# Performance work log

Measured on AMD Instinct MI355X. Metric: run time of the kernel, lower is better.

Reference implementation:

```python
import jax, jax.numpy as jnp
import numpy as np

HID = 1024
VOCAB = 50257
MAXLEN = 2048


def setup_inputs() -> dict:
    key = jax.random.key(0)
    ks = jax.random.split(key, 12)
    s = 0.02
    return {
        "input_tok": jax.random.randint(ks[0], (1,), 0, VOCAB),
        "hidden": jax.random.normal(ks[1], (1, 1, HID), jnp.float32),
        "encoder_outputs": jax.random.normal(ks[2], (MAXLEN, HID), jnp.float32),
        "emb": jax.random.normal(ks[3], (VOCAB, HID), jnp.float32) * s,
        "attn_W": jax.random.normal(ks[4], (MAXLEN, 2 * HID), jnp.float32) * s,
        "attn_b": jnp.zeros((MAXLEN,), jnp.float32),
        "comb_W": jax.random.normal(ks[5], (HID, 2 * HID), jnp.float32) * s,
        "comb_b": jnp.zeros((HID,), jnp.float32),
        "W_ih": jax.random.normal(ks[6], (3 * HID, HID), jnp.float32) * s,
        "W_hh": jax.random.normal(ks[7], (3 * HID, HID), jnp.float32) * s,
        "b_ih": jnp.zeros((3 * HID,), jnp.float32),
        "b_hh": jnp.zeros((3 * HID,), jnp.float32),
        "out_W": jax.random.normal(ks[8], (VOCAB, HID), jnp.float32) * s,
        "out_b": jnp.zeros((VOCAB,), jnp.float32),
    }


def reference(input_tok, hidden, encoder_outputs, emb, attn_W, attn_b,
              comb_W, comb_b, W_ih, W_hh, b_ih, b_hh, out_W, out_b):
    H = hidden.shape[-1]
    # embedding lookup -> [1, H]; dropout is identity in eval mode
    embedded = emb[input_tok].reshape(1, H)
    h = hidden[0]  # [1, H]
    # Bahdanau-style attention over fixed max_length
    attn_weights = jax.nn.softmax(
        jnp.concatenate([embedded, h], axis=1) @ attn_W.T + attn_b, axis=1)  # [1, L]
    attn_applied = attn_weights @ encoder_outputs  # [1, H]
    x = jnp.concatenate([embedded, attn_applied], axis=1) @ comb_W.T + comb_b
    x = jax.nn.relu(x)  # [1, H]
    # single GRU step (PyTorch gate layout: r, z, n)
    gi = x @ W_ih.T + b_ih
    gh = h @ W_hh.T + b_hh
    gi_r, gi_z, gi_n = jnp.split(gi, 3, axis=1)
    gh_r, gh_z, gh_n = jnp.split(gh, 3, axis=1)
    r = jax.nn.sigmoid(gi_r + gh_r)
    z = jax.nn.sigmoid(gi_z + gh_z)
    n = jnp.tanh(gi_n + r * gh_n)
    h_new = (1.0 - z) * n + z * h  # [1, H]
    out = jax.nn.log_softmax(h_new @ out_W.T + out_b, axis=1)  # [1, V]
    return out, h_new[None], attn_weights
```

## Files before the change

### kernel.cpp

```cpp
#include <hip/hip_runtime.h>
#include <math.h>

#define HID    1024
#define VOCAB  50257
#define MAXLEN 2048
#define SMB 256
#define SMR (MAXLEN / SMB)
#define LROWS 32
#define LBLK ((VOCAB + LROWS - 1) / LROWS)

#define WS_SCORES    0
#define WS_APPLIED   4096
#define WS_X         5120
#define WS_GH        6144
#define WS_HNEW      12288
#define WS_PM        16384
#define WS_PS        20480
#define WS_PARTIALS  32768

__device__ inline float wave_reduce_sum(float v) {
    #pragma unroll
    for (int m = 32; m > 0; m >>= 1) v += __shfl_xor(v, m, 64);
    return v;
}

__global__ __launch_bounds__(256) void k_scores_gh(
        const float* __restrict__ emb, const int* __restrict__ tok,
        const float* __restrict__ hidden,
        const float* __restrict__ attn_W, const float* __restrict__ attn_b,
        const float* __restrict__ W_hh, const float* __restrict__ b_hh,
        float* __restrict__ scores, float* __restrict__ gh) {
    int wib = threadIdx.x >> 6, lane = threadIdx.x & 63;
    if (blockIdx.x < 512) {
        int row = blockIdx.x * 4 + wib;
        const float* erow = emb + (size_t)tok[0] * HID;
        const float* wrow = attn_W + (size_t)row * (2 * HID);
        float acc = 0.f;
        #pragma unroll
        for (int i = 0; i < 8; ++i) {
            int k = i * 256 + lane * 4;
            float4 w = *(const float4*)(wrow + k);
            float4 c = (k < HID) ? *(const float4*)(erow + k)
                                 : *(const float4*)(hidden + (k - HID));
            acc += w.x * c.x + w.y * c.y + w.z * c.z + w.w * c.w;
        }
        acc = wave_reduce_sum(acc);
        if (lane == 0) scores[row] = acc + attn_b[row];
    } else {
        int row = (blockIdx.x - 512) * 4 + wib;
        const float* wrow = W_hh + (size_t)row * HID;
        float acc = 0.f;
        #pragma unroll
        for (int i = 0; i < 4; ++i) {
            int k = i * 256 + lane * 4;
            float4 w = *(const float4*)(wrow + k);
            float4 c = *(const float4*)(hidden + k);
            acc += w.x * c.x + w.y * c.y + w.z * c.z + w.w * c.w;
        }
        acc = wave_reduce_sum(acc);
        if (lane == 0) gh[row] = acc + b_hh[row];
    }
}

__global__ __launch_bounds__(256) void k_softmax_apply(
        const float* __restrict__ scores, const float* __restrict__ E,
        float* __restrict__ out_w, float* __restrict__ partials) {
    __shared__ float red[256];
    __shared__ float wrow[SMR];
    int t = threadIdx.x, b = blockIdx.x;
    float v[8];
    float m = -INFINITY;
    #pragma unroll
    for (int i = 0; i < 8; ++i) { v[i] = scores[t + 256 * i]; m = fmaxf(m, v[i]); }
    red[t] = m; __syncthreads();
    for (int s = 128; s > 0; s >>= 1) { if (t < s) red[t] = fmaxf(red[t], red[t + s]); __syncthreads(); }
    float M = red[0]; __syncthreads();
    float s = 0.f;
    #pragma unroll
    for (int i = 0; i < 8; ++i) s += expf(v[i] - M);
    red[t] = s; __syncthreads();
    for (int k = 128; k > 0; k >>= 1) { if (t < k) red[t] += red[t + k]; __syncthreads(); }
    float invS = 1.f / red[0];
    int r0 = b * SMR;
    if (t < SMR) wrow[t] = expf(scores[r0 + t] - M) * invS;
    __syncthreads();
    int j = t * 4;
    float4 acc = make_float4(0.f, 0.f, 0.f, 0.f);
    #pragma unroll
    for (int r = 0; r < SMR; ++r) {
        float w = wrow[r];
        float4 e = *(const float4*)(E + (size_t)(r0 + r) * HID + j);
        acc.x += w * e.x; acc.y += w * e.y; acc.z += w * e.z; acc.w += w * e.w;
    }
    *(float4*)(partials + (size_t)b * HID + j) = acc;
    if (b == 0) {
        #pragma unroll
        for (int i = 0; i < 8; ++i) out_w[t + 256 * i] = expf(v[i] - M) * invS;
    }
}

__global__ __launch_bounds__(256) void k_apply_reduce(
        const float* __restrict__ partials, float* __restrict__ applied) {
    __shared__ float red[256];
    int t = threadIdx.x;
    int co = t & 31, grp = t >> 5;
    int col = blockIdx.x * 32 + co;
    float acc = 0.f;
    #pragma unroll
    for (int cc = 0; cc < 32; ++cc)
        acc += partials[(size_t)(grp * 32 + cc) * HID + col];
    red[grp * 32 + co] = acc;
    __syncthreads();
    if (t < 32) {
        float s = 0.f;
        #pragma unroll
        for (int g = 0; g < 8; ++g) s += red[g * 32 + t];
        applied[blockIdx.x * 32 + t] = s;
    }
}

__global__ __launch_bounds__(256) void k_comb(
        const float* __restrict__ emb, const int* __restrict__ tok,
        const float* __restrict__ applied,
        const float* __restrict__ comb_W, const float* __restrict__ comb_b,
        float* __restrict__ x) {
    int gtid = blockIdx.x * blockDim.x + threadIdx.x;
    int row = gtid >> 6, lane = gtid & 63;
    if (row >= HID) return;
    const float* erow = emb + (size_t)tok[0] * HID;
    const float* wrow = comb_W + (size_t)row * (2 * HID);
    float acc = 0.f;
    #pragma unroll
    for (int i = 0; i < 8; ++i) {
        int k = i * 256 + lane * 4;
        float4 w = *(const float4*)(wrow + k);
        float4 c = (k < HID) ? *(const float4*)(erow + k)
                             : *(const float4*)(applied + (k - HID));
        acc += w.x * c.x + w.y * c.y + w.z * c.z + w.w * c.w;
    }
    acc = wave_reduce_sum(acc);
    if (lane == 0) x[row] = fmaxf(acc + comb_b[row], 0.f);
}

__global__ __launch_bounds__(384) void k_gru_fused(
        const float* __restrict__ W_ih, const float* __restrict__ b_ih,
        const float* __restrict__ x, const float* __restrict__ gh,
        const float* __restrict__ h,
        float* __restrict__ hnew_out, float* __restrict__ hnew_ws) {
    __shared__ float sm[6];
    int w = threadIdx.x >> 6, lane = threadIdx.x & 63;
    int hid = blockIdx.x * 2 + (w >= 3 ? 1 : 0);
    int gate = w % 3;
    int row = gate * HID + hid;
    const float* wrow = W_ih + (size_t)row * HID;
    float acc = 0.f;
    #pragma unroll
    for (int i = 0; i < 4; ++i) {
        int k = i * 256 + lane * 4;
        float4 a = *(const float4*)(wrow + k);
        float4 c = *(const float4*)(x + k);
        acc += a.x * c.x + a.y * c.y + a.z * c.z + a.w * c.w;
    }
    acc = wave_reduce_sum(acc);
    if (lane == 0) sm[w] = acc + b_ih[row];
    __syncthreads();
    if (threadIdx.x == 0 || threadIdx.x == 192) {
        int base = (threadIdx.x == 0) ? 0 : 3;
        int i = blockIdx.x * 2 + (base ? 1 : 0);
        float gir = sm[base + 0], giz = sm[base + 1], gin = sm[base + 2];
        float r = 1.f / (1.f + expf(-(gir + gh[i])));
        float z = 1.f / (1.f + expf(-(giz + gh[i + HID])));
        float n = tanhf(gin + r * gh[i + 2 * HID]);
        float hn = (1.f - z) * n + z * h[i];
        hnew_out[i] = hn;
        hnew_ws[i]  = hn;
    }
}

__global__ __launch_bounds__(512) void k_logits(
        const float* __restrict__ hnew, const float* __restrict__ out_W,
        const float* __restrict__ out_b,
        float* __restrict__ logits, float* __restrict__ pm, float* __restrict__ ps) {
    __shared__ float wm[8], wsum[8];
    int wib = threadIdx.x >> 6, lane = threadIdx.x & 63;
    int r0 = blockIdx.x * LROWS + wib * 4;
    bool val[4]; int rr[4]; const float* wp[4];
    #pragma unroll
    for (int j = 0; j < 4; ++j) {
        val[j] = (r0 + j) < VOCAB;
        rr[j] = val[j] ? (r0 + j) : 0;
        wp[j] = out_W + (size_t)rr[j] * HID;
    }
    float acc[4] = {0.f, 0.f, 0.f, 0.f};
    #pragma unroll
    for (int i = 0; i < 4; ++i) {
        int k = i * 256 + lane * 4;
        float4 c = *(const float4*)(hnew + k);
        #pragma unroll
        for (int j = 0; j < 4; ++j) {
            float4 a = *(const float4*)(wp[j] + k);
            acc[j] += a.x * c.x + a.y * c.y + a.z * c.z + a.w * c.w;
        }
    }
    #pragma unroll
    for (int j = 0; j < 4; ++j) acc[j] = wave_reduce_sum(acc[j]);
    if (lane == 0) {
        float l[4], m = -INFINITY;
        #pragma unroll
        for (int j = 0; j < 4; ++j) {
            l[j] = acc[j] + out_b[rr[j]];
            if (val[j]) { logits[r0 + j] = l[j]; m = fmaxf(m, l[j]); }
        }
        float s = 0.f;
        #pragma unroll
        for (int j = 0; j < 4; ++j) if (val[j]) s += expf(l[j] - m);
        wm[wib] = m; wsum[wib] = s;
    }
    __syncthreads();
    if (threadIdx.x == 0) {
        float M = wm[0];
        #pragma unroll
        for (int i = 1; i < 8; ++i) M = fmaxf(M, wm[i]);
        float S = 0.f;
        #pragma unroll
        for (int i = 0; i < 8; ++i) S += (wsum[i] > 0.f) ? wsum[i] * expf(wm[i] - M) : 0.f;
        pm[blockIdx.x] = M;
        ps[blockIdx.x] = S;
    }
}

__global__ __launch_bounds__(256) void k_logsoftmax_write(
        const float* __restrict__ pm, const float* __restrict__ ps,
        float* __restrict__ out) {
    __shared__ float red[256];
    int t = threadIdx.x;
    float m = -INFINITY;
    for (int i = t; i < LBLK; i += 256) m = fmaxf(m, pm[i]);
    red[t] = m; __syncthreads();
    for (int s = 128; s > 0; s >>= 1) { if (t < s) red[t] = fmaxf(red[t], red[t + s]); __syncthreads(); }
    float M = red[0]; __syncthreads();
    float acc = 0.f;
    for (int i = t; i < LBLK; i += 256) acc += ps[i] * expf(pm[i] - M);
    red[t] = acc; __syncthreads();
    for (int s = 128; s > 0; s >>= 1) { if (t < s) red[t] += red[t + s]; __syncthreads(); }
    float lse = M + logf(red[0]);
    int v = blockIdx.x * 256 + t;
    if (v < VOCAB) out[v] -= lse;
}

extern "C" void kernel_launch(void* const* d_in, const int* in_sizes, int n_in,
                              void* d_out, int out_size, void* d_ws, size_t ws_size,
                              hipStream_t stream) {
    const int*   tok     = (const int*)d_in[0];
    const float* hidden  = (const float*)d_in[1];
    const float* E       = (const float*)d_in[2];
    const float* emb     = (const float*)d_in[3];
    const float* attn_W  = (const float*)d_in[4];
    const float* attn_b  = (const float*)d_in[5];
    const float* comb_W  = (const float*)d_in[6];
    const float* comb_b  = (const float*)d_in[7];
    const float* W_ih    = (const float*)d_in[8];
    const float* W_hh    = (const float*)d_in[9];
    const float* b_ih    = (const float*)d_in[10];
    const float* b_hh    = (const float*)d_in[11];
    const float* out_W   = (const float*)d_in[12];
    const float* out_b   = (const float*)d_in[13];

    float* out       = (float*)d_out;
    float* hnew_out  = out + VOCAB;
    float* attnw_out = out + VOCAB + HID;

    float* ws        = (float*)d_ws;
    float* scores    = ws + WS_SCORES;
    float* applied   = ws + WS_APPLIED;
    float* x         = ws + WS_X;
    float* gh        = ws + WS_GH;
    float* hnew_ws   = ws + WS_HNEW;
    float* pm        = ws + WS_PM;
    float* ps        = ws + WS_PS;
    float* partials  = ws + WS_PARTIALS;

    k_scores_gh<<<1280, 256, 0, stream>>>(emb, tok, hidden, attn_W, attn_b,
                                          W_hh, b_hh, scores, gh);
    k_softmax_apply<<<SMB, 256, 0, stream>>>(scores, E, attnw_out, partials);
    k_apply_reduce<<<32, 256, 0, stream>>>(partials, applied);
    k_comb<<<HID / 4, 256, 0, stream>>>(emb, tok, applied, comb_W, comb_b, x);
    k_gru_fused<<<512, 384, 0, stream>>>(W_ih, b_ih, x, gh, hidden, hnew_out, hnew_ws);
    k_logits<<<LBLK, 512, 0, stream>>>(hnew_ws, out_W, out_b, out, pm, ps);
    k_logsoftmax_write<<<(VOCAB + 255) / 256, 256, 0, stream>>>(pm, ps, out);
}
```

Baseline: 70.17 us.

## Fuse apply-reduce into comb kernel with atomic flag, widen rows per wave

Merges the partial-sum reduction of attention-applied vectors with the combine GEMV into one launch. The combine blocks first compute the embedding half of their dot product, then spin on a global counter until the 32 reducer blocks have published their results. The scores/W_hh and logits GEMVs now have each wave handle 2 and 8 rows respectively, halving block counts. This removes a kernel launch and raises memory-level parallelism per wave, but relies on the reducer blocks being scheduled while the others spin, and uses more registers in the logits kernel.

```diff
diff --git a/kernel.cpp b/kernel.cpp
--- a/kernel.cpp
+++ b/kernel.cpp
@@ -6,7 +6,7 @@
 #define MAXLEN 2048
 #define SMB 256
 #define SMR (MAXLEN / SMB)
-#define LROWS 32
+#define LROWS 64
 #define LBLK ((VOCAB + LROWS - 1) / LROWS)
 
 #define WS_SCORES    0
@@ -14,6 +14,7 @@
 #define WS_X         5120
 #define WS_GH        6144
 #define WS_HNEW      12288
+#define WS_CTR       14336
 #define WS_PM        16384
 #define WS_PS        20480
 #define WS_PARTIALS  32768
@@ -29,36 +30,54 @@
         const float* __restrict__ hidden,
         const float* __restrict__ attn_W, const float* __restrict__ attn_b,
         const float* __restrict__ W_hh, const float* __restrict__ b_hh,
-        float* __restrict__ scores, float* __restrict__ gh) {
+        float* __restrict__ scores, float* __restrict__ gh,
+        unsigned int* __restrict__ ctr) {
+    if (blockIdx.x == 0 && threadIdx.x == 0)
+        __hip_atomic_store(ctr, 0u, __ATOMIC_RELAXED, __HIP_MEMORY_SCOPE_AGENT);
     int wib = threadIdx.x >> 6, lane = threadIdx.x & 63;
-    if (blockIdx.x < 512) {
-        int row = blockIdx.x * 4 + wib;
+    int wtask = blockIdx.x * 4 + wib;
+    if (blockIdx.x < 256) {
+        int r0 = wtask * 2;
         const float* erow = emb + (size_t)tok[0] * HID;
-        const float* wrow = attn_W + (size_t)row * (2 * HID);
-        float acc = 0.f;
+        const float* w0 = attn_W + (size_t)r0 * (2 * HID);
+        const float* w1 = w0 + 2 * HID;
+        float a0 = 0.f, a1 = 0.f;
         #pragma unroll
         for (int i = 0; i < 8; ++i) {
             int k = i * 256 + lane * 4;
-            float4 w = *(const float4*)(wrow + k);
             float4 c = (k < HID) ? *(const float4*)(erow + k)
                                  : *(const float4*)(hidden + (k - HID));
-            acc += w.x * c.x + w.y * c.y + w.z * c.z + w.w * c.w;
-        }
-        acc = wave_reduce_sum(acc);
-        if (lane == 0) scores[row] = acc + attn_b[row];
+            float4 p = *(const float4*)(w0 + k);
+            float4 q = *(const float4*)(w1 + k);
+            a0 += p.x * c.x + p.y * c.y + p.z * c.z + p.w * c.w;
+            a1 += q.x * c.x + q.y * c.y + q.z * c.z + q.w * c.w;
+        }
+        a0 = wave_reduce_sum(a0);
+        a1 = wave_reduce_sum(a1);
+        if (lane == 0) {
+            scores[r0]     = a0 + attn_b[r0];
+            scores[r0 + 1] = a1 + attn_b[r0 + 1];
+        }
     } else {
-        int row = (blockIdx.x - 512) * 4 + wib;
-        const float* wrow = W_hh + (size_t)row * HID;
-        float acc = 0.f;
+        int r0 = (wtask - 1024) * 2;
+        const float* w0 = W_hh + (size_t)r0 * HID;
+        const float* w1 = w0 + HID;
+        float a0 = 0.f, a1 = 0.f;
         #pragma unroll
         for (int i = 0; i < 4; ++i) {
             int k = i * 256 + lane * 4;
-            float4 w = *(const float4*)(wrow + k);
             float4 c = *(const float4*)(hidden + k);
-            acc += w.x * c.x + w.y * c.y + w.z * c.z + w.w * c.w;
-        }
-        acc = wave_reduce_sum(acc);
-        if (lane == 0) gh[row] = acc + b_hh[row];
+            float4 p = *(const float4*)(w0 + k);
+            float4 q = *(const float4*)(w1 + k);
+            a0 += p.x * c.x + p.y * c.y + p.z * c.z + p.w * c.w;
+            a1 += q.x * c.x + q.y * c.y + q.z * c.z + q.w * c.w;
+        }
+        a0 = wave_reduce_sum(a0);
+        a1 = wave_reduce_sum(a1);
+        if (lane == 0) {
+            gh[r0]     = a0 + b_hh[r0];
+            gh[r0 + 1] = a1 + b_hh[r0 + 1];
+        }
     }
 }
 
@@ -99,47 +118,61 @@
     }
 }
 
-__global__ __launch_bounds__(256) void k_apply_reduce(
-        const float* __restrict__ partials, float* __restrict__ applied) {
-    __shared__ float red[256];
-    int t = threadIdx.x;
-    int co = t & 31, grp = t >> 5;
-    int col = blockIdx.x * 32 + co;
-    float acc = 0.f;
-    #pragma unroll
-    for (int cc = 0; cc < 32; ++cc)
-        acc += partials[(size_t)(grp * 32 + cc) * HID + col];
-    red[grp * 32 + co] = acc;
-    __syncthreads();
-    if (t < 32) {
-        float s = 0.f;
-        #pragma unroll
-        for (int g = 0; g < 8; ++g) s += red[g * 32 + t];
-        applied[blockIdx.x * 32 + t] = s;
-    }
-}
-
-__global__ __launch_bounds__(256) void k_comb(
+__global__ __launch_bounds__(256) void k_reduce_comb(
+        const float* __restrict__ partials,
         const float* __restrict__ emb, const int* __restrict__ tok,
-        const float* __restrict__ applied,
         const float* __restrict__ comb_W, const float* __restrict__ comb_b,
-        float* __restrict__ x) {
-    int gtid = blockIdx.x * blockDim.x + threadIdx.x;
-    int row = gtid >> 6, lane = gtid & 63;
-    if (row >= HID) return;
-    const float* erow = emb + (size_t)tok[0] * HID;
-    const float* wrow = comb_W + (size_t)row * (2 * HID);
-    float acc = 0.f;
-    #pragma unroll
-    for (int i = 0; i < 8; ++i) {
-        int k = i * 256 + lane * 4;
-        float4 w = *(const float4*)(wrow + k);
-        float4 c = (k < HID) ? *(const float4*)(erow + k)
-                             : *(const float4*)(applied + (k - HID));
-        acc += w.x * c.x + w.y * c.y + w.z * c.z + w.w * c.w;
-    }
-    acc = wave_reduce_sum(acc);
-    if (lane == 0) x[row] = fmaxf(acc + comb_b[row], 0.f);
+        float* __restrict__ applied, float* __restrict__ x,
+        unsigned int* __restrict__ ctr) {
+    if (blockIdx.x < 32) {
+        __shared__ float red[256];
+        int t = threadIdx.x;
+        int co = t & 31, grp = t >> 5;
+        int col = blockIdx.x * 32 + co;
+        float acc = 0.f;
+        #pragma unroll
+        for (int cc = 0; cc < 32; ++cc)
+            acc += partials[(size_t)(grp * 32 + cc) * HID + col];
+        red[grp * 32 + co] = acc;
+        __syncthreads();
+        if (t < 32) {
+            float s = 0.f;
+            #pragma unroll
+            for (int g = 0; g < 8; ++g) s += red[g * 32 + t];
+            applied[blockIdx.x * 32 + t] = s;
+        }
+        __threadfence();
+        __syncthreads();
+        if (t == 0)
+            __hip_atomic_fetch_add(ctr, 1u, __ATOMIC_RELEASE, __HIP_MEMORY_SCOPE_AGENT);
+    } else {
+        int wib = threadIdx.x >> 6, lane = threadIdx.x & 63;
+        int row = (blockIdx.x - 32) * 4 + wib;
+        const float* erow = emb + (size_t)tok[0] * HID;
+        const float* wrow = comb_W + (size_t)row * (2 * HID);
+        float acc = 0.f;
+        #pragma unroll
+        for (int i = 0; i < 4; ++i) {
+            int k = i * 256 + lane * 4;
+            float4 w = *(const float4*)(wrow + k);
+            float4 c = *(const float4*)(erow + k);
+            acc += w.x * c.x + w.y * c.y + w.z * c.z + w.w * c.w;
+        }
+        if (threadIdx.x == 0) {
+            while (__hip_atomic_load(ctr, __ATOMIC_ACQUIRE, __HIP_MEMORY_SCOPE_AGENT) < 32u)
+                __builtin_amdgcn_s_sleep(2);
+        }
+        __syncthreads();
+        #pragma unroll
+        for (int i = 4; i < 8; ++i) {
+            int k = i * 256 + lane * 4;
+            float4 w = *(const float4*)(wrow + k);
+            float4 c = *(const float4*)(applied + (k - HID));
+            acc += w.x * c.x + w.y * c.y + w.z * c.z + w.w * c.w;
+        }
+        acc = wave_reduce_sum(acc);
+        if (lane == 0) x[row] = fmaxf(acc + comb_b[row], 0.f);
+    }
 }
 
 __global__ __launch_bounds__(384) void k_gru_fused(
@@ -183,37 +216,36 @@
         float* __restrict__ logits, float* __restrict__ pm, float* __restrict__ ps) {
     __shared__ float wm[8], wsum[8];
     int wib = threadIdx.x >> 6, lane = threadIdx.x & 63;
-    int r0 = blockIdx.x * LROWS + wib * 4;
-    bool val[4]; int rr[4]; const float* wp[4];
-    #pragma unroll
-    for (int j = 0; j < 4; ++j) {
+    int r0 = blockIdx.x * LROWS + wib * 8;
+    bool val[8]; int rr[8];
+    #pragma unroll
+    for (int j = 0; j < 8; ++j) {
         val[j] = (r0 + j) < VOCAB;
         rr[j] = val[j] ? (r0 + j) : 0;
-        wp[j] = out_W + (size_t)rr[j] * HID;
-    }
-    float acc[4] = {0.f, 0.f, 0.f, 0.f};
+    }
+    float acc[8] = {0.f, 0.f, 0.f, 0.f, 0.f, 0.f, 0.f, 0.f};
     #pragma unroll
     for (int i = 0; i < 4; ++i) {
         int k = i * 256 + lane * 4;
         float4 c = *(const float4*)(hnew + k);
         #pragma unroll
-        for (int j = 0; j < 4; ++j) {
-            float4 a = *(const float4*)(wp[j] + k);
+        for (int j = 0; j < 8; ++j) {
+            float4 a = *(const float4*)(out_W + (size_t)rr[j] * HID + k);
             acc[j] += a.x * c.x + a.y * c.y + a.z * c.z + a.w * c.w;
         }
     }
     #pragma unroll
-    for (int j = 0; j < 4; ++j) acc[j] = wave_reduce_sum(acc[j]);
+    for (int j = 0; j < 8; ++j) acc[j] = wave_reduce_sum(acc[j]);
     if (lane == 0) {
-        float l[4], m = -INFINITY;
-        #pragma unroll
-        for (int j = 0; j < 4; ++j) {
+        float l[8], m = -INFINITY;
+        #pragma unroll
+        for (int j = 0; j < 8; ++j) {
             l[j] = acc[j] + out_b[rr[j]];
             if (val[j]) { logits[r0 + j] = l[j]; m = fmaxf(m, l[j]); }
         }
         float s = 0.f;
         #pragma unroll
-        for (int j = 0; j < 4; ++j) if (val[j]) s += expf(l[j] - m);
+        for (int j = 0; j < 8; ++j) if (val[j]) s += expf(l[j] - m);
         wm[wib] = m; wsum[wib] = s;
     }
     __syncthreads();
@@ -276,15 +308,16 @@
     float* x         = ws + WS_X;
     float* gh        = ws + WS_GH;
     float* hnew_ws   = ws + WS_HNEW;
+    unsigned int* ctr = (unsigned int*)(ws + WS_CTR);
     float* pm        = ws + WS_PM;
     float* ps        = ws + WS_PS;
     float* partials  = ws + WS_PARTIALS;
 
-    k_scores_gh<<<1280, 256, 0, stream>>>(emb, tok, hidden, attn_W, attn_b,
-                                          W_hh, b_hh, scores, gh);
+    k_scores_gh<<<640, 256, 0, stream>>>(emb, tok, hidden, attn_W, attn_b,
+                                         W_hh, b_hh, scores, gh, ctr);
     k_softmax_apply<<<SMB, 256, 0, stream>>>(scores, E, attnw_out, partials);
-    k_apply_reduce<<<32, 256, 0, stream>>>(partials, applied);
-    k_comb<<<HID / 4, 256, 0, stream>>>(emb, tok, applied, comb_W, comb_b, x);
+    k_reduce_comb<<<288, 256, 0, stream>>>(partials, emb, tok, comb_W, comb_b,
+                                           applied, x, ctr);
     k_gru_fused<<<512, 384, 0, stream>>>(W_ih, b_ih, x, gh, hidden, hnew_out, hnew_ws);
     k_logits<<<LBLK, 512, 0, stream>>>(hnew_ws, out_W, out_b, out, pm, ps);
     k_logsoftmax_write<<<(VOCAB + 255) / 256, 256, 0, stream>>>(pm, ps, out);
```

After: 97.90 us. +39.5%, slower.
